# Kernel tuning notes

Measured on AMD Instinct MI355X. Metric: run time of the kernel, lower is better.

## Reference

```python
import jax, jax.numpy as jnp
import numpy as np

D_MODEL = 2048
NUM_HEADS = 16
NUM_KV_HEADS = 4
HEAD_DIM = D_MODEL // NUM_HEADS
ROPE_THETA = 10000.0


def setup_inputs() -> dict:
    key = jax.random.key(0)
    ks = jax.random.split(key, 5)
    B, S = 2, 2048
    scale = 0.02
    return {
        "x": jax.random.normal(ks[0], (B, S, D_MODEL), dtype=jnp.float32),
        "wq": jax.random.normal(ks[1], (D_MODEL, NUM_HEADS * HEAD_DIM), dtype=jnp.float32) * scale,
        "wk": jax.random.normal(ks[2], (D_MODEL, NUM_KV_HEADS * HEAD_DIM), dtype=jnp.float32) * scale,
        "wv": jax.random.normal(ks[3], (D_MODEL, NUM_KV_HEADS * HEAD_DIM), dtype=jnp.float32) * scale,
        "wo": jax.random.normal(ks[4], (NUM_HEADS * HEAD_DIM, D_MODEL), dtype=jnp.float32) * scale,
    }


def _rope_cos_sin(seq_len, head_dim, dtype):
    # Llama-style: freqs over even indices, angles = pos * inv_freq
    inv_freq = 1.0 / (ROPE_THETA ** (jnp.arange(0, head_dim, 2, dtype=jnp.float32) / head_dim))
    ang = jnp.arange(seq_len, dtype=jnp.float32)[:, None] * inv_freq[None, :]  # [S, hd/2]
    cos = jnp.cos(ang).astype(dtype)[None, :, None, :]  # [1,S,1,hd/2]
    sin = jnp.sin(ang).astype(dtype)[None, :, None, :]
    return cos, sin


def _apply_rope(x, cos, sin):
    # x: [B,S,H,hd]; interleaved complex rotation on pairs (x[2i], x[2i+1])
    x1 = x[..., 0::2]
    x2 = x[..., 1::2]
    y1 = x1 * cos - x2 * sin
    y2 = x1 * sin + x2 * cos
    return jnp.stack([y1, y2], axis=-1).reshape(x.shape)


def reference(x, wq, wk, wv, wo):
    B, S, D = x.shape
    H, KV, hd = NUM_HEADS, NUM_KV_HEADS, HEAD_DIM
    g = H // KV
    q = (x @ wq).reshape(B, S, H, hd)
    k = (x @ wk).reshape(B, S, KV, hd)
    v = (x @ wv).reshape(B, S, KV, hd)
    cos, sin = _rope_cos_sin(S, hd, x.dtype)
    q = _apply_rope(q, cos, sin)
    k = _apply_rope(k, cos, sin)
    q = q.transpose(0, 2, 1, 3)  # [B,H,S,hd]
    k = k.transpose(0, 2, 1, 3)  # [B,KV,S,hd]
    v = v.transpose(0, 2, 1, 3)
    k = jnp.repeat(k, g, axis=1)  # GQA: [B,H,S,hd]
    v = jnp.repeat(v, g, axis=1)
    attn = jnp.einsum('bqsh,bqlh->bqsl', q, k) * (1.0 / np.sqrt(hd)).astype(np.float32)
    attn = jax.nn.softmax(attn, axis=-1)  # non-causal, as in source
    out = jnp.einsum('bqsl,bqlh->bqsh', attn, v)
    out = out.transpose(0, 2, 1, 3).reshape(B, S, D)
    return out @ wo
```

## Files before the change

kernel.cpp:

```cpp
#include <hip/hip_runtime.h>


typedef __attribute__((ext_vector_type(8))) short short8;
typedef __attribute__((ext_vector_type(4))) float f32x4;

#define DEV static __device__ __forceinline__

#define NB 2
#define NS 2048
#define ND 2048
#define NH 16
#define NKV 4
#define HD 128
#define NQKV 3072

DEV unsigned short f2bf(float f) {
  union { float f; unsigned u; } v; v.f = f;
  unsigned r = v.u + 0x7fffu + ((v.u >> 16) & 1u);
  return (unsigned short)(r >> 16);
}
DEV float bf2f(unsigned short u) {
  union { unsigned u; float f; } v; v.u = ((unsigned)u) << 16; return v.f;
}
DEV unsigned pack2bf_rne(float a, float b) {
  return (unsigned)f2bf(a) | ((unsigned)f2bf(b) << 16);
}
DEV unsigned cvtpk(float a, float b) {
  unsigned r;
  asm("v_cvt_pk_bf16_f32 %0, %1, %2" : "=v"(r) : "v"(a), "v"(b));
  return r;
}

DEV void swap32(unsigned &x, unsigned &y) {
  asm volatile("v_permlane32_swap_b32 %0, %1" : "+v"(x), "+v"(y));
}
DEV void swap16(unsigned &x, unsigned &y) {
  asm volatile("v_permlane16_swap_b32 %0, %1" : "+v"(x), "+v"(y));
}

typedef const __attribute__((address_space(1))) void* gas1_t;
typedef __attribute__((address_space(3))) void* las3_t;
DEV void gload16(const void* g, void* l) {
  __builtin_amdgcn_global_load_lds((gas1_t)g, (las3_t)l, 16, 0, 0);
}

DEV f32x4 mfma16(short8 a, short8 b, f32x4 c) {
  return __builtin_amdgcn_mfma_f32_16x16x32_bf16(a, b, c, 0, 0, 0);
}


__global__ __launch_bounds__(256) void convert_x_kernel(const float* __restrict__ x,
                                                        unsigned short* __restrict__ xb) {
  size_t i = ((size_t)blockIdx.x * 256 + threadIdx.x) * 4;
  float4 v = *(const float4*)(x + i);
  unsigned long long pack = (unsigned long long)f2bf(v.x)
                          | ((unsigned long long)f2bf(v.y) << 16)
                          | ((unsigned long long)f2bf(v.z) << 32)
                          | ((unsigned long long)f2bf(v.w) << 48);
  *(unsigned long long*)(xb + i) = pack;
}

__global__ __launch_bounds__(256) void transpose_w_kernel(const float* __restrict__ src,
                                                          unsigned short* __restrict__ dst,
                                                          int K, int N) {
  __shared__ float tile[64][65];
  const int k0 = blockIdx.x * 64, n0 = blockIdx.y * 64;
  for (int i = threadIdx.x; i < 4096; i += 256) {
    int r = i >> 6, c = i & 63;
    tile[r][c] = src[(size_t)(k0 + r) * N + n0 + c];
  }
  __syncthreads();
  for (int i = threadIdx.x; i < 4096; i += 256) {
    int r = i >> 6, c = i & 63;
    dst[(size_t)(n0 + r) * K + k0 + c] = f2bf(tile[c][r]);
  }
}

__global__ __launch_bounds__(256) void rope_table_kernel(float2* __restrict__ tab) {
  int t = blockIdx.x * 256 + threadIdx.x;
  int s = t >> 6, i = t & 63;
  float freq = powf(10000.0f, -(float)i * (1.0f / 64.0f));
  float ang = (float)s * freq;
  tab[t] = make_float2(cosf(ang), sinf(ang));
}

__global__ __launch_bounds__(256) void rope_scatter_kernel(const unsigned short* __restrict__ QKV,
                                                           const float2* __restrict__ tab,
                                                           unsigned short* __restrict__ Qb,
                                                           unsigned short* __restrict__ Kb) {
  int t = blockIdx.x * 256 + threadIdx.x;
  const float qscale = 0.12751741161895452f;
  if (t < (1 << 22)) {
    int i = t & 63, h = (t >> 6) & 15, s = (t >> 10) & 2047, b = t >> 21;
    const unsigned short* p = QKV + (size_t)(b * NS + s) * NQKV + h * HD + 2 * i;
    float2 cs = tab[s * 64 + i];
    float x1 = bf2f(p[0]), x2 = bf2f(p[1]);
    unsigned short* q = Qb + (size_t)((b * NH + h) * NS + s) * HD + 2 * i;
    q[0] = f2bf((x1 * cs.x - x2 * cs.y) * qscale);
    q[1] = f2bf((x1 * cs.y + x2 * cs.x) * qscale);
  } else {
    int u = t - (1 << 22);
    int i = u & 63, kv = (u >> 6) & 3, s = (u >> 8) & 2047, b = u >> 19;
    const unsigned short* p = QKV + (size_t)(b * NS + s) * NQKV + 2048 + kv * HD + 2 * i;
    float2 cs = tab[s * 64 + i];
    float x1 = bf2f(p[0]), x2 = bf2f(p[1]);
    unsigned short* k = Kb + (size_t)((b * NKV + kv) * NS + s) * HD + 2 * i;
    k[0] = f2bf(x1 * cs.x - x2 * cs.y);
    k[1] = f2bf(x1 * cs.y + x2 * cs.x);
  }
}

__global__ __launch_bounds__(256) void transpose_v_kernel(const unsigned short* __restrict__ QKV,
                                                          unsigned short* __restrict__ Vt) {
  __shared__ unsigned short tile[64][65];
  const int bk = blockIdx.x, b = bk >> 2, kv = bk & 3;
  const int s0 = blockIdx.y * 64, d0 = blockIdx.z * 64;
  for (int i = threadIdx.x; i < 4096; i += 256) {
    int r = i >> 6, c = i & 63;
    tile[r][c] = QKV[(size_t)(b * NS + s0 + r) * NQKV + 2560 + kv * HD + d0 + c];
  }
  __syncthreads();
  for (int i = threadIdx.x; i < 4096; i += 256) {
    int r = i >> 6, c = i & 63;
    Vt[(size_t)((b * NKV + kv) * HD + d0 + r) * NS + s0 + c] = tile[c][r];
  }
}


template <int N, bool OUTBF16>
__global__ __launch_bounds__(256) void gemm_kernel(const unsigned short* __restrict__ A,
                                                   const unsigned short* __restrict__ Bt,
                                                   void* __restrict__ Cout) {
  __shared__ unsigned short As[128 * 64];
  __shared__ unsigned short Bs[128 * 64];
  const int K = 2048;
  const int tid = threadIdx.x, wid = tid >> 6, lane = tid & 63;
  const int wm = wid >> 1, wn = wid & 1;

  const int nwg = gridDim.x * gridDim.y;
  const int bid = blockIdx.y * gridDim.x + blockIdx.x;
  const int swzb = (bid & 7) * (nwg >> 3) + (bid >> 3);
  const int m0 = (swzb % gridDim.x) * 128;
  const int n0 = (swzb / gridDim.x) * 128;

  f32x4 acc[4][4] = {};
  const int cl = lane & 15, hi8 = (lane >> 4) * 8;
  const int swg = (cl & 7) << 3;

  const int srow = lane >> 3;
  const int scol = ((lane & 7) * 8) ^ (srow << 3);
  const unsigned short* PA = A + (size_t)(m0 + wid * 8 + srow) * K + scol;
  const unsigned short* PB = Bt + (size_t)(n0 + wid * 8 + srow) * K + scol;

  for (int kt = 0; kt < K; kt += 64) {
#pragma unroll
    for (int i = 0; i < 4; ++i)
      gload16(PA + (size_t)(i * 32) * K + kt, &As[i * 2048 + wid * 512]);
#pragma unroll
    for (int i = 0; i < 4; ++i)
      gload16(PB + (size_t)(i * 32) * K + kt, &Bs[i * 2048 + wid * 512]);
    __syncthreads();

    short8 af[2][4], bfr[2][4];
#pragma unroll
    for (int kk = 0; kk < 2; ++kk) {
#pragma unroll
      for (int r = 0; r < 4; ++r)
        af[kk][r] = *(const short8*)&As[(wm * 64 + r * 16 + cl) * 64 + ((kk * 32 + hi8) ^ swg)];
#pragma unroll
      for (int c = 0; c < 4; ++c)
        bfr[kk][c] = *(const short8*)&Bs[(wn * 64 + c * 16 + cl) * 64 + ((kk * 32 + hi8) ^ swg)];
    }
    __builtin_amdgcn_s_setprio(1);
#pragma unroll
    for (int kk = 0; kk < 2; ++kk)
#pragma unroll
      for (int r = 0; r < 4; ++r)
#pragma unroll
        for (int c = 0; c < 4; ++c)
          acc[r][c] = mfma16(af[kk][r], bfr[kk][c], acc[r][c]);
    __builtin_amdgcn_s_setprio(0);
    __syncthreads();
  }

  if (OUTBF16) {
    unsigned short* C = (unsigned short*)Cout;
#pragma unroll
    for (int r = 0; r < 4; ++r) {
      const int row = m0 + wm * 64 + r * 16 + (lane >> 4) * 4;
#pragma unroll
      for (int c = 0; c < 4; ++c) {
        const int col = n0 + wn * 64 + c * 16 + cl;
#pragma unroll
        for (int j = 0; j < 4; ++j)
          C[(size_t)(row + j) * N + col] = f2bf(acc[r][c][j]);
      }
    }
  } else {
    float* C = (float*)Cout;
#pragma unroll
    for (int r = 0; r < 4; ++r) {
      const int row = m0 + wm * 64 + r * 16 + (lane >> 4) * 4;
#pragma unroll
      for (int c = 0; c < 4; ++c) {
        const int col = n0 + wn * 64 + c * 16 + cl;
#pragma unroll
        for (int j = 0; j < 4; ++j)
          C[(size_t)(row + j) * N + col] = acc[r][c][j];
      }
    }
  }
}


__global__ __launch_bounds__(256, 2) void attn_kernel(const unsigned short* __restrict__ Qb,
                                                      const unsigned short* __restrict__ Kb,
                                                      const unsigned short* __restrict__ Vt,
                                                      unsigned short* __restrict__ O) {
  __shared__ unsigned short Ks[2][64 * 128];
  __shared__ unsigned short Vs[2][128 * 64];
  const int tid = threadIdx.x, wid = tid >> 6, lane = tid & 63;
  const int blk = blockIdx.x;
  const int qt = blk & 15, h = (blk >> 4) & 15, b = blk >> 8;
  const int kvh = h >> 2;
  const int q0 = qt * 128 + wid * 32;

  const unsigned short* qhead = Qb + (size_t)((b * NH + h) * NS) * HD;
  const unsigned short* khead = Kb + (size_t)((b * NKV + kvh) * NS) * HD;
  const unsigned short* vhead = Vt + (size_t)((b * NKV + kvh) * HD) * NS;

  const int cl = lane & 15, g4 = (lane >> 4) * 4, hi8 = (lane >> 4) * 8;
  const int swk = (lane & 7) << 3;

  auto stageKV = [&](int buf, int kt) {
#pragma unroll
    for (int i = 0; i < 4; ++i) {
      int row = i * 16 + (tid >> 4);
      int col = ((tid & 15) * 8) ^ ((row & 7) << 3);
      gload16(khead + (size_t)(kt + row) * HD + col, &Ks[buf][i * 2048 + wid * 512]);
    }
#pragma unroll
    for (int i = 0; i < 4; ++i) {
      int row = i * 32 + (tid >> 3);
      int col = ((tid & 7) * 8) ^ ((row & 7) << 3);
      gload16(vhead + (size_t)row * NS + kt + col, &Vs[buf][i * 2048 + wid * 512]);
    }
  };

  stageKV(0, 0);

  short8 qf[2][4];
#pragma unroll
  for (int r = 0; r < 2; ++r)
#pragma unroll
    for (int kk = 0; kk < 4; ++kk)
      qf[r][kk] = *(const short8*)(qhead + (size_t)(q0 + r * 16 + cl) * HD + kk * 32 + hi8);

  f32x4 od[2][8] = {};
  float mrun[2] = {-1e30f, -1e30f}, lpart[2] = {0.f, 0.f};

  int cur = 0;
  for (int it = 0; it < NS / 64; ++it) {
    if (it + 1 < NS / 64) {
      stageKV(cur ^ 1, (it + 1) * 64);
      asm volatile("s_waitcnt vmcnt(8)" ::: "memory");
    } else {
      asm volatile("s_waitcnt vmcnt(0)" ::: "memory");
    }
    __builtin_amdgcn_s_barrier();

    const unsigned short* ks = Ks[cur];
    const unsigned short* vs = Vs[cur];

    f32x4 s[2][4];
#pragma unroll
    for (int r = 0; r < 2; ++r)
#pragma unroll
      for (int c4 = 0; c4 < 4; ++c4) s[r][c4] = f32x4{0.f, 0.f, 0.f, 0.f};
    __builtin_amdgcn_s_setprio(1);
#pragma unroll
    for (int c4 = 0; c4 < 4; ++c4)
#pragma unroll
      for (int kk = 0; kk < 4; ++kk) {
        short8 kf = *(const short8*)&ks[((c4 * 16 + cl) * 128 + kk * 32 + hi8) ^ swk];
        s[0][c4] = mfma16(kf, qf[0][kk], s[0][c4]);
        s[1][c4] = mfma16(kf, qf[1][kk], s[1][c4]);
      }
    __builtin_amdgcn_s_setprio(0);

    float mt[2];
#pragma unroll
    for (int r = 0; r < 2; ++r) {
      float m = fmaxf(fmaxf(fmaxf(s[r][0][0], s[r][0][1]), fmaxf(s[r][0][2], s[r][0][3])),
                      fmaxf(fmaxf(s[r][1][0], s[r][1][1]), fmaxf(s[r][1][2], s[r][1][3])));
      float m2 = fmaxf(fmaxf(fmaxf(s[r][2][0], s[r][2][1]), fmaxf(s[r][2][2], s[r][2][3])),
                       fmaxf(fmaxf(s[r][3][0], s[r][3][1]), fmaxf(s[r][3][2], s[r][3][3])));
      m = fmaxf(m, m2);
      m = fmaxf(m, __shfl_xor(m, 16, 64));
      m = fmaxf(m, __shfl_xor(m, 32, 64));
      mt[r] = m;
    }
    bool need = (mt[0] > mrun[0] + 8.0f) || (mt[1] > mrun[1] + 8.0f);
    if (__any(need)) {
#pragma unroll
      for (int r = 0; r < 2; ++r) {
        float mn = fmaxf(mrun[r], mt[r]);
        float corr = __builtin_amdgcn_exp2f(mrun[r] - mn);
        mrun[r] = mn;
        lpart[r] *= corr;
#pragma unroll
        for (int c = 0; c < 8; ++c)
          od[r][c] *= corr;
      }
    }
#pragma unroll
    for (int r = 0; r < 2; ++r) {
      float acc = 0.f;
#pragma unroll
      for (int c4 = 0; c4 < 4; ++c4)
#pragma unroll
        for (int j = 0; j < 4; ++j) {
          float p = __builtin_amdgcn_exp2f(s[r][c4][j] - mrun[r]);
          s[r][c4][j] = p;
          acc += p;
        }
      lpart[r] += acc;
    }

    short8 pb[2][2];
#pragma unroll
    for (int r = 0; r < 2; ++r) {
      unsigned w00 = cvtpk(s[r][0][0], s[r][0][1]), w01 = cvtpk(s[r][0][2], s[r][0][3]);
      unsigned w10 = cvtpk(s[r][1][0], s[r][1][1]), w11 = cvtpk(s[r][1][2], s[r][1][3]);
      unsigned w20 = cvtpk(s[r][2][0], s[r][2][1]), w21 = cvtpk(s[r][2][2], s[r][2][3]);
      unsigned w30 = cvtpk(s[r][3][0], s[r][3][1]), w31 = cvtpk(s[r][3][2], s[r][3][3]);
      union { unsigned u[4]; short8 v; } t0, t1;
      swap32(w00, w10); swap16(w00, w10); t0.u[0] = w00; t0.u[2] = w10;
      swap32(w01, w11); swap16(w01, w11); t0.u[1] = w01; t0.u[3] = w11;
      swap32(w20, w30); swap16(w20, w30); t1.u[0] = w20; t1.u[2] = w30;
      swap32(w21, w31); swap16(w21, w31); t1.u[1] = w21; t1.u[3] = w31;
      pb[r][0] = t0.v;
      pb[r][1] = t1.v;
    }

    __builtin_amdgcn_s_setprio(1);
#pragma unroll
    for (int c = 0; c < 8; ++c) {
      const int rr = c * 16 + cl;
      short8 vf0 = *(const short8*)&vs[(rr * 64 + hi8) ^ swk];
      short8 vf1 = *(const short8*)&vs[(rr * 64 + 32 + hi8) ^ swk];
      od[0][c] = mfma16(vf0, pb[0][0], od[0][c]);
      od[0][c] = mfma16(vf1, pb[0][1], od[0][c]);
      od[1][c] = mfma16(vf0, pb[1][0], od[1][c]);
      od[1][c] = mfma16(vf1, pb[1][1], od[1][c]);
    }
    __builtin_amdgcn_s_setprio(0);
    __builtin_amdgcn_s_barrier();
    cur ^= 1;
  }

  float linv[2];
#pragma unroll
  for (int r = 0; r < 2; ++r) {
    float l = lpart[r];
    l += __shfl_xor(l, 16, 64);
    l += __shfl_xor(l, 32, 64);
    linv[r] = 1.0f / l;
  }
#pragma unroll
  for (int r = 0; r < 2; ++r) {
    const size_t row = (size_t)(b * NS + q0 + 16 * r + cl);
#pragma unroll
    for (int c = 0; c < 8; ++c) {
      uint2 pk;
      pk.x = pack2bf_rne(od[r][c][0] * linv[r], od[r][c][1] * linv[r]);
      pk.y = pack2bf_rne(od[r][c][2] * linv[r], od[r][c][3] * linv[r]);
      *(uint2*)(O + row * ND + h * HD + c * 16 + g4) = pk;
    }
  }
}


extern "C" void kernel_launch(void* const* d_in, const int* in_sizes, int n_in,
                              void* d_out, int out_size, void* d_ws, size_t ws_size,
                              hipStream_t stream) {
  const float* x  = (const float*)d_in[0];
  const float* wq = (const float*)d_in[1];
  const float* wk = (const float*)d_in[2];
  const float* wv = (const float*)d_in[3];
  const float* wo = (const float*)d_in[4];
  float* out = (float*)d_out;
  char* ws = (char*)d_ws;

  unsigned short* xb   = (unsigned short*)(ws + 0);
  unsigned short* wT   = (unsigned short*)(ws + 16777216);
  unsigned short* woT  = (unsigned short*)(ws + 29360128);
  float2*         tab  = (float2*)(ws + 37748736);
  unsigned short* QKV  = (unsigned short*)(ws + 38797312);
  unsigned short* Qb   = xb;
  unsigned short* Kb   = wT;
  unsigned short* Vt   = (unsigned short*)(ws + 16777216 + 4194304);
  unsigned short* Obuf = QKV;

  convert_x_kernel<<<8192, 256, 0, stream>>>(x, xb);
  transpose_w_kernel<<<dim3(32, 32), 256, 0, stream>>>(wq, wT, 2048, 2048);
  transpose_w_kernel<<<dim3(32, 8),  256, 0, stream>>>(wk, wT + (size_t)2048 * 2048, 2048, 512);
  transpose_w_kernel<<<dim3(32, 8),  256, 0, stream>>>(wv, wT + (size_t)2560 * 2048, 2048, 512);
  transpose_w_kernel<<<dim3(32, 32), 256, 0, stream>>>(wo, woT, 2048, 2048);
  rope_table_kernel<<<512, 256, 0, stream>>>(tab);

  gemm_kernel<NQKV, true><<<dim3(32, 24), 256, 0, stream>>>(xb, wT, QKV);

  rope_scatter_kernel<<<20480, 256, 0, stream>>>(QKV, tab, Qb, Kb);
  transpose_v_kernel<<<dim3(8, 32, 2), 256, 0, stream>>>(QKV, Vt);

  attn_kernel<<<512, 256, 0, stream>>>(Qb, Kb, Vt, Obuf);

  gemm_kernel<ND, false><<<dim3(32, 16), 256, 0, stream>>>(Obuf, woT, out);
}
```

Baseline: 240.8 us.

## Fuse RoPE and Q/K head scatter into QKV GEMM epilogue; vectorize weight transpose

The QKV GEMM epilogue now applies RoPE, using a lane-pair shuffle to fetch the partner element, and scales Q. It writes Q and K directly in head-major layout and writes V to a compact temporary buffer. This removes the separate rope_scatter kernel and its full round trip of the QKV intermediate. The weight transpose kernel now uses float4 loads and ushort4 stores, and the workspace is re-laid out so woT reuses the wT region after the QKV GEMM. The epilogue does scattered 2-byte stores with table lookups, which may be less coalesced than before.

New measurement: 254.5 us. 5.7% more time.

```diff
diff --git a/kernel.cpp b/kernel.cpp
--- a/kernel.cpp
+++ b/kernel.cpp
@@ -65,14 +65,18 @@
                                                           int K, int N) {
   __shared__ float tile[64][65];
   const int k0 = blockIdx.x * 64, n0 = blockIdx.y * 64;
-  for (int i = threadIdx.x; i < 4096; i += 256) {
-    int r = i >> 6, c = i & 63;
-    tile[r][c] = src[(size_t)(k0 + r) * N + n0 + c];
+  for (int i = threadIdx.x; i < 1024; i += 256) {
+    int r = i >> 4, c4 = (i & 15) * 4;
+    float4 v = *(const float4*)&src[(size_t)(k0 + r) * N + n0 + c4];
+    tile[r][c4] = v.x; tile[r][c4 + 1] = v.y; tile[r][c4 + 2] = v.z; tile[r][c4 + 3] = v.w;
   }
   __syncthreads();
-  for (int i = threadIdx.x; i < 4096; i += 256) {
-    int r = i >> 6, c = i & 63;
-    dst[(size_t)(n0 + r) * K + k0 + c] = f2bf(tile[c][r]);
+  for (int i = threadIdx.x; i < 1024; i += 256) {
+    int rn = i >> 4, k4 = (i & 15) * 4;
+    ushort4 o;
+    o.x = f2bf(tile[k4][rn]);     o.y = f2bf(tile[k4 + 1][rn]);
+    o.z = f2bf(tile[k4 + 2][rn]); o.w = f2bf(tile[k4 + 3][rn]);
+    *(ushort4*)&dst[(size_t)(n0 + rn) * K + k0 + k4] = o;
   }
 }
 
@@ -84,40 +88,14 @@
   tab[t] = make_float2(cosf(ang), sinf(ang));
 }
 
-__global__ __launch_bounds__(256) void rope_scatter_kernel(const unsigned short* __restrict__ QKV,
-                                                           const float2* __restrict__ tab,
-                                                           unsigned short* __restrict__ Qb,
-                                                           unsigned short* __restrict__ Kb) {
-  int t = blockIdx.x * 256 + threadIdx.x;
-  const float qscale = 0.12751741161895452f;
-  if (t < (1 << 22)) {
-    int i = t & 63, h = (t >> 6) & 15, s = (t >> 10) & 2047, b = t >> 21;
-    const unsigned short* p = QKV + (size_t)(b * NS + s) * NQKV + h * HD + 2 * i;
-    float2 cs = tab[s * 64 + i];
-    float x1 = bf2f(p[0]), x2 = bf2f(p[1]);
-    unsigned short* q = Qb + (size_t)((b * NH + h) * NS + s) * HD + 2 * i;
-    q[0] = f2bf((x1 * cs.x - x2 * cs.y) * qscale);
-    q[1] = f2bf((x1 * cs.y + x2 * cs.x) * qscale);
-  } else {
-    int u = t - (1 << 22);
-    int i = u & 63, kv = (u >> 6) & 3, s = (u >> 8) & 2047, b = u >> 19;
-    const unsigned short* p = QKV + (size_t)(b * NS + s) * NQKV + 2048 + kv * HD + 2 * i;
-    float2 cs = tab[s * 64 + i];
-    float x1 = bf2f(p[0]), x2 = bf2f(p[1]);
-    unsigned short* k = Kb + (size_t)((b * NKV + kv) * NS + s) * HD + 2 * i;
-    k[0] = f2bf(x1 * cs.x - x2 * cs.y);
-    k[1] = f2bf(x1 * cs.y + x2 * cs.x);
-  }
-}
-
-__global__ __launch_bounds__(256) void transpose_v_kernel(const unsigned short* __restrict__ QKV,
+__global__ __launch_bounds__(256) void transpose_v_kernel(const unsigned short* __restrict__ Vtmp,
                                                           unsigned short* __restrict__ Vt) {
   __shared__ unsigned short tile[64][65];
   const int bk = blockIdx.x, b = bk >> 2, kv = bk & 3;
   const int s0 = blockIdx.y * 64, d0 = blockIdx.z * 64;
   for (int i = threadIdx.x; i < 4096; i += 256) {
     int r = i >> 6, c = i & 63;
-    tile[r][c] = QKV[(size_t)(b * NS + s0 + r) * NQKV + 2560 + kv * HD + d0 + c];
+    tile[r][c] = Vtmp[(size_t)(b * NS + s0 + r) * 512 + kv * 128 + d0 + c];
   }
   __syncthreads();
   for (int i = threadIdx.x; i < 4096; i += 256) {
@@ -127,10 +105,14 @@
 }
 
 
-template <int N, bool OUTBF16>
+template <int N, int MODE>
 __global__ __launch_bounds__(256) void gemm_kernel(const unsigned short* __restrict__ A,
                                                    const unsigned short* __restrict__ Bt,
-                                                   void* __restrict__ Cout) {
+                                                   float* __restrict__ Cout,
+                                                   const float2* __restrict__ tab,
+                                                   unsigned short* __restrict__ Qb,
+                                                   unsigned short* __restrict__ Kb,
+                                                   unsigned short* __restrict__ Vtmp) {
   __shared__ unsigned short As[128 * 64];
   __shared__ unsigned short Bs[128 * 64];
   const int K = 2048;
@@ -183,8 +165,8 @@
     __syncthreads();
   }
 
-  if (OUTBF16) {
-    unsigned short* C = (unsigned short*)Cout;
+  if constexpr (MODE == 0) {
+    float* C = Cout;
 #pragma unroll
     for (int r = 0; r < 4; ++r) {
       const int row = m0 + wm * 64 + r * 16 + (lane >> 4) * 4;
@@ -193,20 +175,51 @@
         const int col = n0 + wn * 64 + c * 16 + cl;
 #pragma unroll
         for (int j = 0; j < 4; ++j)
-          C[(size_t)(row + j) * N + col] = f2bf(acc[r][c][j]);
+          C[(size_t)(row + j) * N + col] = acc[r][c][j];
       }
     }
   } else {
-    float* C = (float*)Cout;
-#pragma unroll
-    for (int r = 0; r < 4; ++r) {
-      const int row = m0 + wm * 64 + r * 16 + (lane >> 4) * 4;
-#pragma unroll
-      for (int c = 0; c < 4; ++c) {
-        const int col = n0 + wn * 64 + c * 16 + cl;
-#pragma unroll
-        for (int j = 0; j < 4; ++j)
-          C[(size_t)(row + j) * N + col] = acc[r][c][j];
+    const int coltile = n0 >> 7;
+    if (coltile < 20) {
+      const bool isQ = (coltile < 16);
+      const int hh = isQ ? coltile : (coltile - 16);
+      const int heads = isQ ? NH : NKV;
+      unsigned short* Dst = isQ ? Qb : Kb;
+      const float qsc = 0.12751741161895452f;
+      const float sgn = (lane & 1) ? 1.0f : -1.0f;
+#pragma unroll
+      for (int r = 0; r < 4; ++r) {
+        const int row0 = m0 + wm * 64 + r * 16 + (lane >> 4) * 4;
+#pragma unroll
+        for (int c = 0; c < 4; ++c) {
+          const int d = wn * 64 + c * 16 + cl;
+          const int ii = d >> 1;
+          float p[4];
+#pragma unroll
+          for (int j = 0; j < 4; ++j) p[j] = __shfl_xor(acc[r][c][j], 1, 64);
+#pragma unroll
+          for (int j = 0; j < 4; ++j) {
+            const int row = row0 + j;
+            const int s = row & (NS - 1), bb = row >> 11;
+            float2 cs = tab[s * 64 + ii];
+            float o = acc[r][c][j] * cs.x + p[j] * cs.y * sgn;
+            if (isQ) o *= qsc;
+            Dst[((size_t)(bb * heads + hh) * NS + s) * HD + d] = f2bf(o);
+          }
+        }
+      }
+    } else {
+      const int vc = (coltile - 20) * 128;
+#pragma unroll
+      for (int r = 0; r < 4; ++r) {
+        const int row0 = m0 + wm * 64 + r * 16 + (lane >> 4) * 4;
+#pragma unroll
+        for (int c = 0; c < 4; ++c) {
+          const int d = wn * 64 + c * 16 + cl;
+#pragma unroll
+          for (int j = 0; j < 4; ++j)
+            Vtmp[(size_t)(row0 + j) * 512 + vc + d] = f2bf(acc[r][c][j]);
+        }
       }
     }
   }
@@ -394,27 +407,26 @@
 
   unsigned short* xb   = (unsigned short*)(ws + 0);
   unsigned short* wT   = (unsigned short*)(ws + 16777216);
-  unsigned short* woT  = (unsigned short*)(ws + 29360128);
-  float2*         tab  = (float2*)(ws + 37748736);
-  unsigned short* QKV  = (unsigned short*)(ws + 38797312);
-  unsigned short* Qb   = xb;
-  unsigned short* Kb   = wT;
-  unsigned short* Vt   = (unsigned short*)(ws + 16777216 + 4194304);
-  unsigned short* Obuf = QKV;
+  float2*         tab  = (float2*)(ws + 29360128);
+  unsigned short* Qb   = (unsigned short*)(ws + 30408704);
+  unsigned short* Kb   = (unsigned short*)(ws + 47185920);
+  unsigned short* Vtmp = (unsigned short*)(ws + 51380224);
+  unsigned short* Vt   = (unsigned short*)(ws + 55574528);
+  unsigned short* woT  = wT;
+  unsigned short* Obuf = xb;
 
   convert_x_kernel<<<8192, 256, 0, stream>>>(x, xb);
   transpose_w_kernel<<<dim3(32, 32), 256, 0, stream>>>(wq, wT, 2048, 2048);
   transpose_w_kernel<<<dim3(32, 8),  256, 0, stream>>>(wk, wT + (size_t)2048 * 2048, 2048, 512);
   transpose_w_kernel<<<dim3(32, 8),  256, 0, stream>>>(wv, wT + (size_t)2560 * 2048, 2048, 512);
+  rope_table_kernel<<<512, 256, 0, stream>>>(tab);
+
+  gemm_kernel<NQKV, 1><<<dim3(32, 24), 256, 0, stream>>>(xb, wT, nullptr, tab, Qb, Kb, Vtmp);
+
   transpose_w_kernel<<<dim3(32, 32), 256, 0, stream>>>(wo, woT, 2048, 2048);
-  rope_table_kernel<<<512, 256, 0, stream>>>(tab);
-
-  gemm_kernel<NQKV, true><<<dim3(32, 24), 256, 0, stream>>>(xb, wT, QKV);
-
-  rope_scatter_kernel<<<20480, 256, 0, stream>>>(QKV, tab, Qb, Kb);
-  transpose_v_kernel<<<dim3(8, 32, 2), 256, 0, stream>>>(QKV, Vt);
+  transpose_v_kernel<<<dim3(8, 32, 2), 256, 0, stream>>>(Vtmp, Vt);
 
   attn_kernel<<<512, 256, 0, stream>>>(Qb, Kb, Vt, Obuf);
 
-  gemm_kernel<ND, false><<<dim3(32, 16), 256, 0, stream>>>(Obuf, woT, out);
-}
+  gemm_kernel<ND, 0><<<dim3(32, 16), 256, 0, stream>>>(Obuf, woT, out, nullptr, nullptr, nullptr, nullptr);
+}
```

## Replace GEMM with 256x256-tile double-buffered pipelined kernel and vectorize weight transpose

Applied to the files above, without the earlier changes.

The GEMM moves from 128x128 tiles with 4 waves to 256x256 tiles with 8 waves. It double-buffers LDS and issues next-tile global-to-LDS loads in quarter phases, overlapped with MFMA on the current buffer through partial vmcnt waits. This raises arithmetic intensity and hides load latency, but it also cuts the grid size to 192 and 128 workgroups, which may underfill the 256 CUs. The weight transpose kernel separately switches to float4 loads and ushort4 stores.

New measurement: 243.4 us. No clear change (+1.1%).

```diff
diff --git a/kernel.cpp b/kernel.cpp
--- a/kernel.cpp
+++ b/kernel.cpp
@@ -65,14 +65,18 @@
                                                           int K, int N) {
   __shared__ float tile[64][65];
   const int k0 = blockIdx.x * 64, n0 = blockIdx.y * 64;
-  for (int i = threadIdx.x; i < 4096; i += 256) {
-    int r = i >> 6, c = i & 63;
-    tile[r][c] = src[(size_t)(k0 + r) * N + n0 + c];
+  for (int i = threadIdx.x; i < 1024; i += 256) {
+    int r = i >> 4, c4 = (i & 15) * 4;
+    float4 v = *(const float4*)&src[(size_t)(k0 + r) * N + n0 + c4];
+    tile[r][c4] = v.x; tile[r][c4 + 1] = v.y; tile[r][c4 + 2] = v.z; tile[r][c4 + 3] = v.w;
   }
   __syncthreads();
-  for (int i = threadIdx.x; i < 4096; i += 256) {
-    int r = i >> 6, c = i & 63;
-    dst[(size_t)(n0 + r) * K + k0 + c] = f2bf(tile[c][r]);
+  for (int i = threadIdx.x; i < 1024; i += 256) {
+    int rn = i >> 4, k4 = (i & 15) * 4;
+    ushort4 o;
+    o.x = f2bf(tile[k4][rn]);     o.y = f2bf(tile[k4 + 1][rn]);
+    o.z = f2bf(tile[k4 + 2][rn]); o.w = f2bf(tile[k4 + 3][rn]);
+    *(ushort4*)&dst[(size_t)(n0 + rn) * K + k0 + k4] = o;
   }
 }
 
@@ -128,85 +132,117 @@
 
 
 template <int N, bool OUTBF16>
-__global__ __launch_bounds__(256) void gemm_kernel(const unsigned short* __restrict__ A,
-                                                   const unsigned short* __restrict__ Bt,
-                                                   void* __restrict__ Cout) {
-  __shared__ unsigned short As[128 * 64];
-  __shared__ unsigned short Bs[128 * 64];
-  const int K = 2048;
+__global__ __launch_bounds__(512) void gemm256_kernel(const unsigned short* __restrict__ A,
+                                                      const unsigned short* __restrict__ Bt,
+                                                      void* __restrict__ Cout) {
+  __shared__ unsigned short Sm[2][2][2][256 * 32];
+  const int K = 2048, NT = K / 64;
   const int tid = threadIdx.x, wid = tid >> 6, lane = tid & 63;
-  const int wm = wid >> 1, wn = wid & 1;
+  const int wm = wid >> 2, wn = wid & 3;
 
   const int nwg = gridDim.x * gridDim.y;
   const int bid = blockIdx.y * gridDim.x + blockIdx.x;
   const int swzb = (bid & 7) * (nwg >> 3) + (bid >> 3);
-  const int m0 = (swzb % gridDim.x) * 128;
-  const int n0 = (swzb / gridDim.x) * 128;
-
-  f32x4 acc[4][4] = {};
-  const int cl = lane & 15, hi8 = (lane >> 4) * 8;
-  const int swg = (cl & 7) << 3;
-
-  const int srow = lane >> 3;
-  const int scol = ((lane & 7) * 8) ^ (srow << 3);
-  const unsigned short* PA = A + (size_t)(m0 + wid * 8 + srow) * K + scol;
-  const unsigned short* PB = Bt + (size_t)(n0 + wid * 8 + srow) * K + scol;
-
-  for (int kt = 0; kt < K; kt += 64) {
-#pragma unroll
-    for (int i = 0; i < 4; ++i)
-      gload16(PA + (size_t)(i * 32) * K + kt, &As[i * 2048 + wid * 512]);
-#pragma unroll
-    for (int i = 0; i < 4; ++i)
-      gload16(PB + (size_t)(i * 32) * K + kt, &Bs[i * 2048 + wid * 512]);
-    __syncthreads();
-
-    short8 af[2][4], bfr[2][4];
-#pragma unroll
-    for (int kk = 0; kk < 2; ++kk) {
-#pragma unroll
-      for (int r = 0; r < 4; ++r)
-        af[kk][r] = *(const short8*)&As[(wm * 64 + r * 16 + cl) * 64 + ((kk * 32 + hi8) ^ swg)];
-#pragma unroll
-      for (int c = 0; c < 4; ++c)
-        bfr[kk][c] = *(const short8*)&Bs[(wn * 64 + c * 16 + cl) * 64 + ((kk * 32 + hi8) ^ swg)];
-    }
-    __builtin_amdgcn_s_setprio(1);
-#pragma unroll
-    for (int kk = 0; kk < 2; ++kk)
-#pragma unroll
-      for (int r = 0; r < 4; ++r)
-#pragma unroll
-        for (int c = 0; c < 4; ++c)
-          acc[r][c] = mfma16(af[kk][r], bfr[kk][c], acc[r][c]);
-    __builtin_amdgcn_s_setprio(0);
-    __syncthreads();
+  const int m0 = (swzb % gridDim.x) * 256;
+  const int n0 = (swzb / gridDim.x) * 256;
+
+  const int cl = lane & 15, g = lane >> 4;
+  const int rsw = (cl & 3) << 3;
+
+  const int stg_row = tid >> 2;
+  const int stg_colE = ((tid & 3) * 8) ^ ((stg_row & 3) << 3);
+  const unsigned short* Abase = A + (size_t)(m0 + stg_row) * K + stg_colE;
+  const unsigned short* Bbase = Bt + (size_t)(n0 + stg_row) * K + stg_colE;
+
+  auto stage_half = [&](int buf, int kt, int h) {
+    const int op = h & 1, kh = h >> 1;
+    const unsigned short* s0 = (op ? Bbase : Abase) + kt + kh * 32;
+    unsigned short* dst = &Sm[buf][op][kh][wid * 512];
+    gload16(s0, dst);
+    gload16(s0 + (size_t)128 * K, dst + 4096);
+  };
+
+  auto read_a = [&](int buf, int kh, int r) -> short8 {
+    const int row = wm * 128 + r * 16 + cl;
+    return *(const short8*)&Sm[buf][0][kh][row * 32 + ((g * 8) ^ rsw)];
+  };
+  auto read_b = [&](int buf, int kh, int cf) -> short8 {
+    const int row = wn * 64 + cf * 16 + cl;
+    return *(const short8*)&Sm[buf][1][kh][row * 32 + ((g * 8) ^ rsw)];
+  };
+
+  f32x4 acc[8][4] = {};
+  short8 af[8];
+
+#pragma unroll
+  for (int h = 0; h < 4; ++h) stage_half(0, 0, h);
+
+  for (int t = 0; t < NT - 1; ++t) {
+    const int buf = t & 1, ktn = (t + 1) * 64;
+#pragma unroll
+    for (int ph = 0; ph < 4; ++ph) {
+      stage_half(buf ^ 1, ktn, ph);
+      asm volatile("s_waitcnt vmcnt(6)" ::: "memory");
+      __builtin_amdgcn_s_barrier();
+      const int kh = ph >> 1, ch = ph & 1;
+      if (ch == 0) {
+#pragma unroll
+        for (int r = 0; r < 8; ++r) af[r] = read_a(buf, kh, r);
+      }
+      short8 b0 = read_b(buf, kh, ch * 2);
+      short8 b1 = read_b(buf, kh, ch * 2 + 1);
+      __builtin_amdgcn_s_setprio(1);
+#pragma unroll
+      for (int r = 0; r < 8; ++r) {
+        acc[r][ch * 2]     = mfma16(af[r], b0, acc[r][ch * 2]);
+        acc[r][ch * 2 + 1] = mfma16(af[r], b1, acc[r][ch * 2 + 1]);
+      }
+      __builtin_amdgcn_s_setprio(0);
+      __builtin_amdgcn_s_barrier();
+    }
+  }
+
+  asm volatile("s_waitcnt vmcnt(0)" ::: "memory");
+  __builtin_amdgcn_s_barrier();
+  {
+    const int buf = (NT - 1) & 1;
+#pragma unroll
+    for (int kh = 0; kh < 2; ++kh) {
+#pragma unroll
+      for (int r = 0; r < 8; ++r) af[r] = read_a(buf, kh, r);
+#pragma unroll
+      for (int cf = 0; cf < 4; ++cf) {
+        short8 b = read_b(buf, kh, cf);
+#pragma unroll
+        for (int r = 0; r < 8; ++r) acc[r][cf] = mfma16(af[r], b, acc[r][cf]);
+      }
+    }
   }
 
   if (OUTBF16) {
     unsigned short* C = (unsigned short*)Cout;
 #pragma unroll
-    for (int r = 0; r < 4; ++r) {
-      const int row = m0 + wm * 64 + r * 16 + (lane >> 4) * 4;
-#pragma unroll
-      for (int c = 0; c < 4; ++c) {
-        const int col = n0 + wn * 64 + c * 16 + cl;
+    for (int r = 0; r < 8; ++r) {
+      const int row0 = m0 + wm * 128 + r * 16 + g * 4;
+#pragma unroll
+      for (int cf = 0; cf < 4; ++cf) {
+        const int col = n0 + wn * 64 + cf * 16 + cl;
 #pragma unroll
         for (int j = 0; j < 4; ++j)
-          C[(size_t)(row + j) * N + col] = f2bf(acc[r][c][j]);
+          C[(size_t)(row0 + j) * N + col] = f2bf(acc[r][cf][j]);
       }
     }
   } else {
     float* C = (float*)Cout;
 #pragma unroll
-    for (int r = 0; r < 4; ++r) {
-      const int row = m0 + wm * 64 + r * 16 + (lane >> 4) * 4;
-#pragma unroll
-      for (int c = 0; c < 4; ++c) {
-        const int col = n0 + wn * 64 + c * 16 + cl;
+    for (int r = 0; r < 8; ++r) {
+      const int row0 = m0 + wm * 128 + r * 16 + g * 4;
+#pragma unroll
+      for (int cf = 0; cf < 4; ++cf) {
+        const int col = n0 + wn * 64 + cf * 16 + cl;
 #pragma unroll
         for (int j = 0; j < 4; ++j)
-          C[(size_t)(row + j) * N + col] = acc[r][c][j];
+          C[(size_t)(row0 + j) * N + col] = acc[r][cf][j];
       }
     }
   }
@@ -409,12 +445,12 @@
   transpose_w_kernel<<<dim3(32, 32), 256, 0, stream>>>(wo, woT, 2048, 2048);
   rope_table_kernel<<<512, 256, 0, stream>>>(tab);
 
-  gemm_kernel<NQKV, true><<<dim3(32, 24), 256, 0, stream>>>(xb, wT, QKV);
+  gemm256_kernel<NQKV, true><<<dim3(16, 12), 512, 0, stream>>>(xb, wT, QKV);
 
   rope_scatter_kernel<<<20480, 256, 0, stream>>>(QKV, tab, Qb, Kb);
   transpose_v_kernel<<<dim3(8, 32, 2), 256, 0, stream>>>(QKV, Vt);
 
   attn_kernel<<<512, 256, 0, stream>>>(Qb, Kb, Vt, Obuf);
 
-  gemm_kernel<ND, false><<<dim3(32, 16), 256, 0, stream>>>(Obuf, woT, out);
-}
+  gemm256_kernel<ND, false><<<dim3(16, 8), 512, 0, stream>>>(Obuf, woT, out);
+}
```
